# Performance work log

Measured on AMD Instinct MI355X. Metric: run time of the kernel, lower is better.

Reference implementation:

```python
import jax, jax.numpy as jnp
import numpy as np

B, J, FIN, FOUT = 8192, 17, 128, 128
BN_EPS = 1e-5


def setup_inputs() -> dict:
    key = jax.random.key(0)
    k_x, k_w, k_adj, k_b = jax.random.split(key, 4)
    x = jax.random.normal(k_x, (B, J, FIN), dtype=jnp.float32)
    # Xavier-uniform-ish init for W [2, FIN, FOUT]
    limit = 1.414 * np.sqrt(6.0 / (FIN + FOUT))
    W = jax.random.uniform(k_w, (2, FIN, FOUT), minval=-limit, maxval=limit, dtype=jnp.float32)
    M = jnp.ones((J, FOUT), dtype=jnp.float32)
    # binary-ish skeleton adjacency buffer (constant)
    adj = (jax.random.uniform(k_adj, (J, J)) > 0.7).astype(jnp.float32)
    adj = adj + jnp.eye(J, dtype=jnp.float32)  # self loops like skeleton graphs
    adj2 = jnp.full((J, J), 1e-6, dtype=jnp.float32)
    stdv = 1.0 / np.sqrt(FOUT)
    bias = jax.random.uniform(k_b, (FOUT,), minval=-stdv, maxval=stdv, dtype=jnp.float32)
    gamma = jnp.ones((FOUT,), dtype=jnp.float32)
    beta = jnp.zeros((FOUT,), dtype=jnp.float32)
    return {"x": x, "W": W, "M": M, "adj": adj, "adj2": adj2,
            "bias": bias, "gamma": gamma, "beta": beta}


def reference(x, W, M, adj, adj2, bias, gamma, beta):
    # ModulatedGraphConv
    h0 = jnp.einsum('bjf,fo->bjo', x, W[0])
    h1 = jnp.einsum('bjf,fo->bjo', x, W[1])
    a = adj + adj2
    a = (a.T + a) * 0.5                       # symmetrize [J, J]
    diag = jnp.diagonal(a)                    # [J]
    off = a * (1.0 - jnp.eye(a.shape[0], dtype=a.dtype))  # zero diagonal
    # diag part: adj*E is diagonal -> per-node scaling; off-diag: dense matmul over J
    out = diag[None, :, None] * (M * h0) + jnp.einsum('ij,bjo->bio', off, M * h1)
    out = out + bias[None, None, :]           # [B, J, FOUT]
    # BatchNorm1d over channel dim (training-mode batch stats over B and J)
    mean = out.mean(axis=(0, 1))
    var = out.var(axis=(0, 1))                # biased variance, as torch BN uses
    out = (out - mean) * jax.lax.rsqrt(var + BN_EPS) * gamma + beta
    return jax.nn.relu(out)
```

## Files before the change

kernel.cpp:

```cpp
#include <hip/hip_runtime.h>


#define NSLOT      128
#define OFF_PART   0
#define OFF_STATS  32768
#define OFF_OFFSYM 33024
#define OFF_DIAG   33364
#define OFF_WBT    33408
#define OFF_PRE    49792
#define PRE_SHORTS (139264ull * 128ull)

typedef __attribute__((ext_vector_type(8))) short bf16x8;
typedef __attribute__((ext_vector_type(4))) short bf16x4;
typedef __attribute__((ext_vector_type(4))) float f32x4;
typedef union { unsigned u[2]; bf16x4 v; } pk4U;

__device__ __forceinline__ short f2bf(float f) {
    unsigned u = __float_as_uint(f);
    u += 0x7FFFu + ((u >> 16) & 1u);
    return (short)(u >> 16);
}
__device__ __forceinline__ float bf2f(short h) {
    return __uint_as_float(((unsigned)(unsigned short)h) << 16);
}
__device__ __forceinline__ float bflo(int p) {
    return __uint_as_float(((unsigned)p) << 16);
}
__device__ __forceinline__ float bfhi(int p) {
    return __uint_as_float(((unsigned)p) & 0xFFFF0000u);
}
__device__ __forceinline__ unsigned pk2(float a, float b) {
    unsigned r;
    asm("v_cvt_pk_bf16_f32 %0, %1, %2" : "=v"(r) : "v"(a), "v"(b));
    return r;
}

__global__ __launch_bounds__(256) void prep_kernel(
    const float* __restrict__ W, const float* __restrict__ adj,
    const float* __restrict__ adj2, float* __restrict__ wsf)
{
    const int t = threadIdx.x, b = blockIdx.x;
    if (b == 0) {
        for (int e = t; e < 340; e += 256) {
            int i = e / 20, j = e % 20;
            float v = 0.f;
            if (j < 17) {
                v = 0.5f * (adj[i*17+j] + adj2[i*17+j] + adj[j*17+i] + adj2[j*17+i]);
                if (i == j) { wsf[OFF_DIAG + i] = v; v = 0.f; }
            }
            wsf[OFF_OFFSYM + e] = v;
        }
        return;
    }
    short* wbt = (short*)(wsf + OFF_WBT);
    const int col = (b - 1) * 16 + (t >> 4);
    const int k0  = (t & 15) * 8;
    const int sel = col >> 7, colp = col & 127;
    const float* src = W + sel * 16384 + colp;
    bf16x8 p;
    #pragma unroll
    for (int e = 0; e < 8; ++e) p[e] = f2bf(src[(k0 + e) * 128]);
    *(bf16x8*)(wbt + col * 128 + k0) = p;
}

template<int USE_BF16>
__global__ __launch_bounds__(512, 4) void conv_kernel(
    const float* __restrict__ x, const float* __restrict__ M,
    const float* __restrict__ bias, float* ws,
    float* __restrict__ out, short* __restrict__ pre)
{
    __shared__ int hhI[68 * 130];
    __shared__ __align__(16) float offs[340];
    short (*A)[136] = (short(*)[136])hhI;

    const int tid = threadIdx.x;
    const int w = tid >> 6, l = tid & 63, c = l & 15, g = l >> 4;

    for (int e = tid; e < 340; e += 512) offs[e] = ws[OFF_OFFSYM + e];

    const float4* xsrc = (const float4*)(x + (size_t)blockIdx.x * (68 * 128));
    #pragma unroll
    for (int it = 0; it < 5; ++it) {
        int f = tid + it * 512;
        if (f < 2176) {
            float4 v = xsrc[f];
            int r = f >> 5, k0 = (f & 31) << 2;
            pk4U p;
            p.u[0] = pk2(v.x, v.y);
            p.u[1] = pk2(v.z, v.w);
            *(bf16x4*)&A[r][k0] = p.v;
        }
    }
    if (tid < 408) {
        bf16x4 z = {0, 0, 0, 0};
        ((bf16x4*)&A[68][0])[tid] = z;
    }
    __syncthreads();

    const short* wbt = (const short*)(ws + OFF_WBT);
    const int col = w * 16 + c;
    f32x4 acc0[5], acc1[5];
    #pragma unroll
    for (int mt = 0; mt < 5; ++mt) {
        acc0[mt] = (f32x4){0.f, 0.f, 0.f, 0.f};
        acc1[mt] = (f32x4){0.f, 0.f, 0.f, 0.f};
    }
    #pragma unroll
    for (int ks = 0; ks < 4; ++ks) {
        bf16x8 b0 = *(const bf16x8*)(wbt + col * 128 + ks * 32 + g * 8);
        bf16x8 b1 = *(const bf16x8*)(wbt + (col + 128) * 128 + ks * 32 + g * 8);
        #pragma unroll
        for (int mt = 0; mt < 5; ++mt) {
            bf16x8 af = *(const bf16x8*)&A[mt * 16 + c][ks * 32 + g * 8];
            acc0[mt] = __builtin_amdgcn_mfma_f32_16x16x32_bf16(af, b0, acc0[mt], 0, 0, 0);
            acc1[mt] = __builtin_amdgcn_mfma_f32_16x16x32_bf16(af, b1, acc1[mt], 0, 0, 0);
        }
    }
    __syncthreads();

    const float bv = bias[col];
    #pragma unroll
    for (int mt = 0; mt < 5; ++mt) {
        #pragma unroll
        for (int r = 0; r < 4; ++r) {
            int row = mt * 16 + g * 4 + r;
            if (row < 68) {
                int j = row - 17 * ((row * 241) >> 12);
                float m  = M[j * 128 + col];
                float dg = ws[OFF_DIAG + j];
                float lo = fmaf(dg * m, acc0[mt][r], bv);
                float hi = m * acc1[mt][r];
                hhI[row * 130 + col] = (int)pk2(lo, hi);
            }
        }
    }
    __syncthreads();

    const int bb = tid >> 7, o = tid & 127;
    const int rb = bb * 17;
    int pj[17];
    #pragma unroll
    for (int i = 0; i < 17; ++i) pj[i] = hhI[(rb + i) * 130 + o];

    float vout[17];
    #pragma unroll
    for (int q = 0; q < 17; ++q) vout[q] = bflo(pj[q]);
    #pragma unroll
    for (int j = 0; j < 17; ++j) {
        float h1v = bfhi(pj[j]);
        const f32x4* orow = (const f32x4*)&offs[j * 20];
        f32x4 o0 = orow[0], o1 = orow[1], o2 = orow[2], o3 = orow[3];
        float oz = offs[j * 20 + 16];
        vout[0]  = fmaf(o0.x, h1v, vout[0]);
        vout[1]  = fmaf(o0.y, h1v, vout[1]);
        vout[2]  = fmaf(o0.z, h1v, vout[2]);
        vout[3]  = fmaf(o0.w, h1v, vout[3]);
        vout[4]  = fmaf(o1.x, h1v, vout[4]);
        vout[5]  = fmaf(o1.y, h1v, vout[5]);
        vout[6]  = fmaf(o1.z, h1v, vout[6]);
        vout[7]  = fmaf(o1.w, h1v, vout[7]);
        vout[8]  = fmaf(o2.x, h1v, vout[8]);
        vout[9]  = fmaf(o2.y, h1v, vout[9]);
        vout[10] = fmaf(o2.z, h1v, vout[10]);
        vout[11] = fmaf(o2.w, h1v, vout[11]);
        vout[12] = fmaf(o3.x, h1v, vout[12]);
        vout[13] = fmaf(o3.y, h1v, vout[13]);
        vout[14] = fmaf(o3.z, h1v, vout[14]);
        vout[15] = fmaf(o3.w, h1v, vout[15]);
        vout[16] = fmaf(oz,   h1v, vout[16]);
    }

    float s = 0.f, s2 = 0.f;
    const size_t gbase = ((size_t)blockIdx.x * 68 + rb) * 128 + o;
    #pragma unroll
    for (int q = 0; q < 17; ++q) {
        float v = vout[q];
        if (USE_BF16) pre[gbase + (size_t)q * 128] = (short)pk2(v, v);
        else          out[gbase + (size_t)q * 128] = v;
        s += v; s2 = fmaf(v, v, s2);
    }

    float* slot = ws + OFF_PART + ((blockIdx.x & (NSLOT - 1)) << 8);
    atomicAdd(slot + o, s);
    atomicAdd(slot + 128 + o, s2);
}

__global__ __launch_bounds__(256) void bn_reduce_kernel(
    const float* __restrict__ part, const float* __restrict__ gamma,
    const float* __restrict__ beta, float* __restrict__ stats)
{
    const int t = threadIdx.x;
    float s = 0.f;
    #pragma unroll 8
    for (int i = 0; i < NSLOT; ++i) s += part[i * 256 + t];
    __shared__ float tot[256];
    tot[t] = s;
    __syncthreads();
    if (t < 128) {
        const float n = 139264.f;
        float mean = tot[t] / n;
        float var  = tot[t + 128] / n - mean * mean;
        var = fmaxf(var, 0.f);
        float inv = rsqrtf(var + 1e-5f);
        float sc = gamma[t] * inv;
        stats[t] = sc;
        stats[t + 128] = beta[t] - mean * sc;
    }
}

__global__ __launch_bounds__(256) void apply_bf16_kernel(
    const short* __restrict__ pre, const float* __restrict__ stats,
    float* __restrict__ out)
{
    const int tid = blockIdx.x * 256 + threadIdx.x;
    const int c0 = (tid << 3) & 127;
    float sc[8], sh[8];
    #pragma unroll
    for (int e = 0; e < 8; ++e) { sc[e] = stats[c0 + e]; sh[e] = stats[128 + c0 + e]; }
    const bf16x8* p8 = (const bf16x8*)pre;
    for (int q = tid; q < 2228224; q += 524288) {
        bf16x8 v = p8[q];
        float4 o0, o1;
        o0.x = fmaxf(fmaf(bf2f(v[0]), sc[0], sh[0]), 0.f);
        o0.y = fmaxf(fmaf(bf2f(v[1]), sc[1], sh[1]), 0.f);
        o0.z = fmaxf(fmaf(bf2f(v[2]), sc[2], sh[2]), 0.f);
        o0.w = fmaxf(fmaf(bf2f(v[3]), sc[3], sh[3]), 0.f);
        o1.x = fmaxf(fmaf(bf2f(v[4]), sc[4], sh[4]), 0.f);
        o1.y = fmaxf(fmaf(bf2f(v[5]), sc[5], sh[5]), 0.f);
        o1.z = fmaxf(fmaf(bf2f(v[6]), sc[6], sh[6]), 0.f);
        o1.w = fmaxf(fmaf(bf2f(v[7]), sc[7], sh[7]), 0.f);
        float4* dst = (float4*)(out + (size_t)q * 8);
        dst[0] = o0; dst[1] = o1;
    }
}

__global__ __launch_bounds__(256) void apply_kernel(
    float* __restrict__ out, const float* __restrict__ stats, int n4)
{
    const int tid = blockIdx.x * 256 + threadIdx.x;
    const int c0 = (tid << 2) & 127;
    const float sc0 = stats[c0],     sc1 = stats[c0 + 1],
                sc2 = stats[c0 + 2], sc3 = stats[c0 + 3];
    const float sh0 = stats[128 + c0],     sh1 = stats[128 + c0 + 1],
                sh2 = stats[128 + c0 + 2], sh3 = stats[128 + c0 + 3];
    float4* o4 = (float4*)out;
    for (int q = tid; q < n4; q += 2048 * 256) {
        float4 v = o4[q];
        v.x = fmaxf(fmaf(v.x, sc0, sh0), 0.f);
        v.y = fmaxf(fmaf(v.y, sc1, sh1), 0.f);
        v.z = fmaxf(fmaf(v.z, sc2, sh2), 0.f);
        v.w = fmaxf(fmaf(v.w, sc3, sh3), 0.f);
        o4[q] = v;
    }
}

extern "C" void kernel_launch(void* const* d_in, const int* in_sizes, int n_in,
                              void* d_out, int out_size, void* d_ws, size_t ws_size,
                              hipStream_t stream) {
    (void)in_sizes; (void)n_in; (void)out_size;
    const float* x     = (const float*)d_in[0];
    const float* W     = (const float*)d_in[1];
    const float* M     = (const float*)d_in[2];
    const float* adj   = (const float*)d_in[3];
    const float* adj2  = (const float*)d_in[4];
    const float* bias  = (const float*)d_in[5];
    const float* gamma = (const float*)d_in[6];
    const float* beta  = (const float*)d_in[7];
    float* out = (float*)d_out;
    float* wsf = (float*)d_ws;
    short* pre = (short*)(wsf + OFF_PRE);

    const bool big = ws_size >= (size_t)OFF_PRE * 4 + PRE_SHORTS * 2;

    (void)hipMemsetAsync(d_ws, 0, NSLOT * 256 * sizeof(float), stream);
    prep_kernel<<<17, 256, 0, stream>>>(W, adj, adj2, wsf);
    if (big) {
        conv_kernel<1><<<2048, 512, 0, stream>>>(x, M, bias, wsf, out, pre);
        bn_reduce_kernel<<<1, 256, 0, stream>>>(wsf + OFF_PART, gamma, beta, wsf + OFF_STATS);
        apply_bf16_kernel<<<2048, 256, 0, stream>>>(pre, wsf + OFF_STATS, out);
    } else {
        conv_kernel<0><<<2048, 512, 0, stream>>>(x, M, bias, wsf, out, pre);
        bn_reduce_kernel<<<1, 256, 0, stream>>>(wsf + OFF_PART, gamma, beta, wsf + OFF_STATS);
        apply_kernel<<<2048, 256, 0, stream>>>(out, wsf + OFF_STATS, 4456448);
    }
}
```

Baseline: 80.32 us.

## Split fused conv into separate GEMM and graph-mix kernels via global scratch

The fused conv kernel is split in the bf16 path into a GEMM kernel and a separate mix kernel. The GEMM kernel writes packed bf16 h0/h1 pairs into the output buffer, which serves as scratch. The mix kernel then applies M, diag, bias and the 17x17 off-diagonal adjacency mix, and accumulates the BN partial sums. This lowers LDS use and the syncs per block, which may improve occupancy. The cost is an extra round trip of about 18 MB through global memory, one more launch, and bf16 rounding of h before the M scaling.

```diff
diff --git a/kernel.cpp b/kernel.cpp
--- a/kernel.cpp
+++ b/kernel.cpp
@@ -63,20 +63,12 @@
     *(bf16x8*)(wbt + col * 128 + k0) = p;
 }
 
-template<int USE_BF16>
-__global__ __launch_bounds__(512, 4) void conv_kernel(
-    const float* __restrict__ x, const float* __restrict__ M,
-    const float* __restrict__ bias, float* ws,
-    float* __restrict__ out, short* __restrict__ pre)
-{
-    __shared__ int hhI[68 * 130];
-    __shared__ __align__(16) float offs[340];
-    short (*A)[136] = (short(*)[136])hhI;
-
+__global__ __launch_bounds__(512, 4) void gemm_kernel(
+    const float* __restrict__ x, const float* ws, int* __restrict__ hh)
+{
+    __shared__ short A[80][136];
     const int tid = threadIdx.x;
     const int w = tid >> 6, l = tid & 63, c = l & 15, g = l >> 4;
-
-    for (int e = tid; e < 340; e += 512) offs[e] = ws[OFF_OFFSYM + e];
 
     const float4* xsrc = (const float4*)(x + (size_t)blockIdx.x * (68 * 128));
     #pragma unroll
@@ -116,8 +108,128 @@
             acc1[mt] = __builtin_amdgcn_mfma_f32_16x16x32_bf16(af, b1, acc1[mt], 0, 0, 0);
         }
     }
-    __syncthreads();
-
+
+    int* dst = hh + (size_t)blockIdx.x * (68 * 128);
+    #pragma unroll
+    for (int mt = 0; mt < 5; ++mt) {
+        #pragma unroll
+        for (int r = 0; r < 4; ++r) {
+            int row = mt * 16 + g * 4 + r;
+            if (row < 68) {
+                unsigned pk = ((unsigned)(unsigned short)f2bf(acc0[mt][r])) |
+                              (((unsigned)(unsigned short)f2bf(acc1[mt][r])) << 16);
+                dst[row * 128 + col] = (int)pk;
+            }
+        }
+    }
+}
+
+__global__ __launch_bounds__(256, 4) void mix_kernel(
+    const int* __restrict__ hh, const float* __restrict__ M,
+    const float* __restrict__ bias, float* ws, short* __restrict__ pre)
+{
+    __shared__ __align__(16) float offs[340];
+    __shared__ float dlds[17];
+    const int tid = threadIdx.x;
+    for (int e = tid; e < 340; e += 256) offs[e] = ws[OFF_OFFSYM + e];
+    if (tid < 17) dlds[tid] = ws[OFF_DIAG + tid];
+    __syncthreads();
+
+    const int o = tid & 127;
+    const size_t b = (size_t)blockIdx.x * 2 + (tid >> 7);
+    const float bv = bias[o];
+    float mcol[17];
+    #pragma unroll
+    for (int j = 0; j < 17; ++j) mcol[j] = M[j * 128 + o];
+
+    const size_t base = b * (17 * 128) + o;
+    int pj[17];
+    #pragma unroll
+    for (int i = 0; i < 17; ++i) pj[i] = hh[base + (size_t)i * 128];
+
+    float vout[17];
+    #pragma unroll
+    for (int i = 0; i < 17; ++i)
+        vout[i] = fmaf(dlds[i] * mcol[i], bflo(pj[i]), bv);
+    #pragma unroll
+    for (int j = 0; j < 17; ++j) {
+        float hv = mcol[j] * bfhi(pj[j]);
+        const f32x4* orow = (const f32x4*)&offs[j * 20];
+        f32x4 o0 = orow[0], o1 = orow[1], o2 = orow[2], o3 = orow[3];
+        float oz = offs[j * 20 + 16];
+        vout[0]  = fmaf(o0.x, hv, vout[0]);
+        vout[1]  = fmaf(o0.y, hv, vout[1]);
+        vout[2]  = fmaf(o0.z, hv, vout[2]);
+        vout[3]  = fmaf(o0.w, hv, vout[3]);
+        vout[4]  = fmaf(o1.x, hv, vout[4]);
+        vout[5]  = fmaf(o1.y, hv, vout[5]);
+        vout[6]  = fmaf(o1.z, hv, vout[6]);
+        vout[7]  = fmaf(o1.w, hv, vout[7]);
+        vout[8]  = fmaf(o2.x, hv, vout[8]);
+        vout[9]  = fmaf(o2.y, hv, vout[9]);
+        vout[10] = fmaf(o2.z, hv, vout[10]);
+        vout[11] = fmaf(o2.w, hv, vout[11]);
+        vout[12] = fmaf(o3.x, hv, vout[12]);
+        vout[13] = fmaf(o3.y, hv, vout[13]);
+        vout[14] = fmaf(o3.z, hv, vout[14]);
+        vout[15] = fmaf(o3.w, hv, vout[15]);
+        vout[16] = fmaf(oz,   hv, vout[16]);
+    }
+
+    float s = 0.f, s2 = 0.f;
+    #pragma unroll
+    for (int i = 0; i < 17; ++i) {
+        float v = vout[i];
+        pre[base + (size_t)i * 128] = (short)pk2(v, v);
+        s += v; s2 = fmaf(v, v, s2);
+    }
+    float* slot = ws + OFF_PART + ((blockIdx.x & (NSLOT - 1)) << 8);
+    atomicAdd(slot + o, s);
+    atomicAdd(slot + 128 + o, s2);
+}
+
+__global__ __launch_bounds__(512, 4) void conv_f32_kernel(
+    const float* __restrict__ x, const float* __restrict__ M,
+    const float* __restrict__ bias, float* ws, float* __restrict__ out)
+{
+    __shared__ int hhI[68 * 130];
+    __shared__ __align__(16) float offs[340];
+    short (*A)[136] = (short(*)[136])hhI;
+    const int tid = threadIdx.x;
+    const int w = tid >> 6, l = tid & 63, c = l & 15, g = l >> 4;
+    for (int e = tid; e < 340; e += 512) offs[e] = ws[OFF_OFFSYM + e];
+    const float4* xsrc = (const float4*)(x + (size_t)blockIdx.x * (68 * 128));
+    #pragma unroll
+    for (int it = 0; it < 5; ++it) {
+        int f = tid + it * 512;
+        if (f < 2176) {
+            float4 v = xsrc[f];
+            int r = f >> 5, k0 = (f & 31) << 2;
+            pk4U p; p.u[0] = pk2(v.x, v.y); p.u[1] = pk2(v.z, v.w);
+            *(bf16x4*)&A[r][k0] = p.v;
+        }
+    }
+    if (tid < 408) { bf16x4 z = {0,0,0,0}; ((bf16x4*)&A[68][0])[tid] = z; }
+    __syncthreads();
+    const short* wbt = (const short*)(ws + OFF_WBT);
+    const int col = w * 16 + c;
+    f32x4 acc0[5], acc1[5];
+    #pragma unroll
+    for (int mt = 0; mt < 5; ++mt) {
+        acc0[mt] = (f32x4){0.f,0.f,0.f,0.f}; acc1[mt] = (f32x4){0.f,0.f,0.f,0.f};
+    }
+    #pragma unroll
+    for (int ks = 0; ks < 4; ++ks) {
+        bf16x8 b0 = *(const bf16x8*)(wbt + col * 128 + ks * 32 + g * 8);
+        bf16x8 b1 = *(const bf16x8*)(wbt + (col + 128) * 128 + ks * 32 + g * 8);
+        #pragma unroll
+        for (int mt = 0; mt < 5; ++mt) {
+            bf16x8 af = *(const bf16x8*)&A[mt * 16 + c][ks * 32 + g * 8];
+            acc0[mt] = __builtin_amdgcn_mfma_f32_16x16x32_bf16(af, b0, acc0[mt], 0, 0, 0);
+            acc1[mt] = __builtin_amdgcn_mfma_f32_16x16x32_bf16(af, b1, acc1[mt], 0, 0, 0);
+        }
+    }
+    __syncthreads();
     const float bv = bias[col];
     #pragma unroll
     for (int mt = 0; mt < 5; ++mt) {
@@ -135,51 +247,28 @@
         }
     }
     __syncthreads();
-
     const int bb = tid >> 7, o = tid & 127;
     const int rb = bb * 17;
     int pj[17];
     #pragma unroll
     for (int i = 0; i < 17; ++i) pj[i] = hhI[(rb + i) * 130 + o];
-
     float vout[17];
     #pragma unroll
     for (int q = 0; q < 17; ++q) vout[q] = bflo(pj[q]);
     #pragma unroll
     for (int j = 0; j < 17; ++j) {
         float h1v = bfhi(pj[j]);
-        const f32x4* orow = (const f32x4*)&offs[j * 20];
-        f32x4 o0 = orow[0], o1 = orow[1], o2 = orow[2], o3 = orow[3];
-        float oz = offs[j * 20 + 16];
-        vout[0]  = fmaf(o0.x, h1v, vout[0]);
-        vout[1]  = fmaf(o0.y, h1v, vout[1]);
-        vout[2]  = fmaf(o0.z, h1v, vout[2]);
-        vout[3]  = fmaf(o0.w, h1v, vout[3]);
-        vout[4]  = fmaf(o1.x, h1v, vout[4]);
-        vout[5]  = fmaf(o1.y, h1v, vout[5]);
-        vout[6]  = fmaf(o1.z, h1v, vout[6]);
-        vout[7]  = fmaf(o1.w, h1v, vout[7]);
-        vout[8]  = fmaf(o2.x, h1v, vout[8]);
-        vout[9]  = fmaf(o2.y, h1v, vout[9]);
-        vout[10] = fmaf(o2.z, h1v, vout[10]);
-        vout[11] = fmaf(o2.w, h1v, vout[11]);
-        vout[12] = fmaf(o3.x, h1v, vout[12]);
-        vout[13] = fmaf(o3.y, h1v, vout[13]);
-        vout[14] = fmaf(o3.z, h1v, vout[14]);
-        vout[15] = fmaf(o3.w, h1v, vout[15]);
-        vout[16] = fmaf(oz,   h1v, vout[16]);
-    }
-
+        #pragma unroll
+        for (int q = 0; q < 17; ++q) vout[q] = fmaf(offs[j * 20 + q], h1v, vout[q]);
+    }
     float s = 0.f, s2 = 0.f;
     const size_t gbase = ((size_t)blockIdx.x * 68 + rb) * 128 + o;
     #pragma unroll
     for (int q = 0; q < 17; ++q) {
         float v = vout[q];
-        if (USE_BF16) pre[gbase + (size_t)q * 128] = (short)pk2(v, v);
-        else          out[gbase + (size_t)q * 128] = v;
+        out[gbase + (size_t)q * 128] = v;
         s += v; s2 = fmaf(v, v, s2);
     }
-
     float* slot = ws + OFF_PART + ((blockIdx.x & (NSLOT - 1)) << 8);
     atomicAdd(slot + o, s);
     atomicAdd(slot + 128 + o, s2);
@@ -275,11 +364,12 @@
     (void)hipMemsetAsync(d_ws, 0, NSLOT * 256 * sizeof(float), stream);
     prep_kernel<<<17, 256, 0, stream>>>(W, adj, adj2, wsf);
     if (big) {
-        conv_kernel<1><<<2048, 512, 0, stream>>>(x, M, bias, wsf, out, pre);
+        gemm_kernel<<<2048, 512, 0, stream>>>(x, wsf, (int*)d_out);
+        mix_kernel<<<4096, 256, 0, stream>>>((const int*)d_out, M, bias, wsf, pre);
         bn_reduce_kernel<<<1, 256, 0, stream>>>(wsf + OFF_PART, gamma, beta, wsf + OFF_STATS);
         apply_bf16_kernel<<<2048, 256, 0, stream>>>(pre, wsf + OFF_STATS, out);
     } else {
-        conv_kernel<0><<<2048, 512, 0, stream>>>(x, M, bias, wsf, out, pre);
+        conv_f32_kernel<<<2048, 512, 0, stream>>>(x, M, bias, wsf, out);
         bn_reduce_kernel<<<1, 256, 0, stream>>>(wsf + OFF_PART, gamma, beta, wsf + OFF_STATS);
         apply_kernel<<<2048, 256, 0, stream>>>(out, wsf + OFF_STATS, 4456448);
     }
```

Result: slower. 93.34 us (+16.2%).
